# Kernel optimization log

Hardware: AMD Instinct MI355X
Metric: run time of the kernel (lower is better)

Reference implementation:

```python
import jax, jax.numpy as jnp
import numpy as np

B, S, D, H, E, N = 4, 1024, 1024, 4096, 1024, 8


def setup_inputs() -> dict:
    key = jax.random.key(0)
    ks = jax.random.split(key, 5)
    x = jax.random.normal(ks[0], (B, S, D), jnp.float32)
    # Learned parameters (Linear weights stored as [in, out] for x @ W)
    Wg = jax.random.normal(ks[1], (D, N), jnp.float32) * 0.02
    bg = jnp.zeros((N,), jnp.float32)
    W1 = jax.random.normal(ks[2], (N, D, H), jnp.float32) * 0.02
    b1 = jnp.zeros((N, H), jnp.float32)
    W2 = jax.random.normal(ks[3], (N, H, E), jnp.float32) * 0.02
    b2 = jnp.zeros((N, E), jnp.float32)
    return {"x": x, "Wg": Wg, "bg": bg, "W1": W1, "b1": b1,
            "W2": W2, "b2": b2, "num_experts_per_tok": 2}


def reference(x, Wg, bg, W1, b1, W2, b2, num_experts_per_tok):
    # Gating: softmax over experts
    gate_probs = jax.nn.softmax(x @ Wg + bg, axis=-1)            # [B,S,N]
    n_exp = gate_probs.shape[-1]
    # Top-k routing mask (indices are distinct, so summed one-hots == scatter of 1.0)
    _, topk_idx = jax.lax.top_k(gate_probs, num_experts_per_tok)  # [B,S,k]
    mask = jax.nn.one_hot(topk_idx, n_exp, dtype=gate_probs.dtype).sum(axis=-2)  # [B,S,N]
    gated = gate_probs * mask
    # F.normalize(p=1): divide by max(L1-norm, eps)
    gated = gated / jnp.maximum(jnp.sum(jnp.abs(gated), axis=-1, keepdims=True), 1e-12)
    # Dense all-expert FFN (matches torch.stack over ModuleList)
    h = jax.nn.relu(jnp.einsum('bsd,ndh->bsnh', x, W1) + b1)      # [B,S,N,H]
    expert_out = jnp.einsum('bsnh,nhe->bsne', h, W2) + b2          # [B,S,N,E]
    out = jnp.einsum('bsn,bsne->bse', gated, expert_out)           # [B,S,E]
    # Auxiliary load-balancing stats
    tokens = float(x.shape[0] * x.shape[1])
    importance = gate_probs.sum(axis=(0, 1)) / tokens              # [N]
    load = mask.sum(axis=(0, 1)) / tokens                          # [N]
    lb_loss = (n_exp * (importance * load).sum()).astype(out.dtype)
    return out, lb_loss, importance, load
```

## Files before the change

kernel.cpp:

```cpp
#include <hip/hip_runtime.h>

#define TOKENS 4096
#define DDIM 1024
#define HDIM 4096
#define EDIM 1024
#define NEXP 8
#define SLOTS (TOKENS * 2)
#define OUT_MAIN ((size_t)TOKENS * EDIM)
#define NKC2 2
#define KCHUNK2 (HDIM / NKC2)

typedef __bf16 bf16_t;
typedef bf16_t bf16x8 __attribute__((ext_vector_type(8)));
typedef float f32x4 __attribute__((ext_vector_type(4)));

__device__ __forceinline__ unsigned short f32_to_bf16(float f) {
  union { float f; unsigned u; } v; v.f = f;
  unsigned r = v.u + 0x7FFFu + ((v.u >> 16) & 1u);
  return (unsigned short)(r >> 16);
}

__device__ __forceinline__ void gload_lds16(const void* g, void* l) {
  __builtin_amdgcn_global_load_lds(
      (__attribute__((address_space(1))) void*)(g),
      (__attribute__((address_space(3))) void*)(l), 16, 0, 0);
}

__global__ __launch_bounds__(256) void gate_kernel(
    const float* __restrict__ x, const float* __restrict__ Wg,
    const float* __restrict__ bg, unsigned short* __restrict__ xb,
    int2* __restrict__ tok_e, float2* __restrict__ tok_w,
    float* __restrict__ probs) {
  const int wave = threadIdx.x >> 6;
  const int lane = threadIdx.x & 63;
  const int t = blockIdx.x * 4 + wave;
  const float4* xr = reinterpret_cast<const float4*>(x + (size_t)t * DDIM);
  ushort4* xbr = reinterpret_cast<ushort4*>(xb + (size_t)t * DDIM);

  float acc[NEXP];
#pragma unroll
  for (int n = 0; n < NEXP; n++) acc[n] = 0.f;

#pragma unroll
  for (int i = 0; i < 4; i++) {
    int d4 = lane + 64 * i;
    float4 xv = xr[d4];
    ushort4 o;
    o.x = f32_to_bf16(xv.x); o.y = f32_to_bf16(xv.y);
    o.z = f32_to_bf16(xv.z); o.w = f32_to_bf16(xv.w);
    xbr[d4] = o;
    const float* wrow = Wg + (size_t)d4 * 4 * NEXP;
#pragma unroll
    for (int n = 0; n < NEXP; n++)
      acc[n] += xv.x * wrow[n] + xv.y * wrow[NEXP + n] +
                xv.z * wrow[2 * NEXP + n] + xv.w * wrow[3 * NEXP + n];
  }
#pragma unroll
  for (int n = 0; n < NEXP; n++)
#pragma unroll
    for (int m = 32; m > 0; m >>= 1) acc[n] += __shfl_xor(acc[n], m, 64);

  if (lane == 0) {
    float p[NEXP];
    float mx = -1e30f;
#pragma unroll
    for (int n = 0; n < NEXP; n++) { p[n] = acc[n] + bg[n]; mx = fmaxf(mx, p[n]); }
    float s = 0.f;
#pragma unroll
    for (int n = 0; n < NEXP; n++) { p[n] = expf(p[n] - mx); s += p[n]; }
    float inv = 1.f / s;
#pragma unroll
    for (int n = 0; n < NEXP; n++) { p[n] *= inv; probs[(size_t)t * NEXP + n] = p[n]; }
    int e1 = 0; float p1 = p[0];
#pragma unroll
    for (int n = 1; n < NEXP; n++) if (p[n] > p1) { p1 = p[n]; e1 = n; }
    int e2 = (e1 == 0) ? 1 : 0; float p2 = p[e2];
#pragma unroll
    for (int n = 0; n < NEXP; n++) if (n != e1 && p[n] > p2) { p2 = p[n]; e2 = n; }
    float denom = p1 + p2;
    tok_e[t] = make_int2(e1, e2);
    tok_w[t] = make_float2(p1 / denom, p2 / denom);
  }
}

__global__ __launch_bounds__(1024) void route_kernel(
    const int2* __restrict__ tok_e, const float2* __restrict__ tok_w,
    int* __restrict__ offs_g, int* __restrict__ counts_g,
    int* __restrict__ token_ids, float* __restrict__ slot_w) {
  __shared__ int cnt[NEXP];
  __shared__ int offs[NEXP + 1];
  __shared__ int cur[NEXP];
  const int tid = threadIdx.x;
  if (tid < NEXP) cnt[tid] = 0;
  __syncthreads();
  int2 e[4]; float2 w[4];
#pragma unroll
  for (int i = 0; i < 4; i++) {
    int t = tid + 1024 * i;
    e[i] = tok_e[t]; w[i] = tok_w[t];
    atomicAdd(&cnt[e[i].x], 1);
    atomicAdd(&cnt[e[i].y], 1);
  }
  __syncthreads();
  if (tid == 0) {
    int s = 0;
#pragma unroll
    for (int n = 0; n < NEXP; n++) { offs[n] = s; cur[n] = s; s += cnt[n]; }
    offs[NEXP] = s;
  }
  __syncthreads();
  if (tid < NEXP) { offs_g[tid] = offs[tid]; counts_g[tid] = cnt[tid]; }
  if (tid == 0) offs_g[NEXP] = offs[NEXP];
#pragma unroll
  for (int i = 0; i < 4; i++) {
    int t = tid + 1024 * i;
    int s0 = atomicAdd(&cur[e[i].x], 1);
    token_ids[s0] = t; slot_w[s0] = w[i].x;
    int s1 = atomicAdd(&cur[e[i].y], 1);
    token_ids[s1] = t; slot_w[s1] = w[i].y;
  }
}

__global__ __launch_bounds__(256) void transpose_convert_kernel(
    const float* __restrict__ src, unsigned short* __restrict__ dst, int R, int C) {
  __shared__ float tile[64][65];
  const size_t mat = (size_t)R * C;
  const float* s = src + (size_t)blockIdx.z * mat;
  unsigned short* d = dst + (size_t)blockIdx.z * mat;
  int c0 = blockIdx.x * 64, r0 = blockIdx.y * 64;
  int tx = threadIdx.x & 15, ty = threadIdx.x >> 4;
#pragma unroll
  for (int i = 0; i < 4; i++) {
    int row = ty + 16 * i;
    float4 v = *reinterpret_cast<const float4*>(&s[(size_t)(r0 + row) * C + c0 + tx * 4]);
    tile[row][tx * 4 + 0] = v.x;
    tile[row][tx * 4 + 1] = v.y;
    tile[row][tx * 4 + 2] = v.z;
    tile[row][tx * 4 + 3] = v.w;
  }
  __syncthreads();
#pragma unroll
  for (int i = 0; i < 4; i++) {
    int col = ty + 16 * i;
    ushort4 o;
    o.x = f32_to_bf16(tile[tx * 4 + 0][col]);
    o.y = f32_to_bf16(tile[tx * 4 + 1][col]);
    o.z = f32_to_bf16(tile[tx * 4 + 2][col]);
    o.w = f32_to_bf16(tile[tx * 4 + 3][col]);
    *reinterpret_cast<ushort4*>(&d[(size_t)(c0 + col) * R + r0 + tx * 4]) = o;
  }
}

__global__ __launch_bounds__(256) void gemm1_kernel(
    const unsigned short* __restrict__ xb, const unsigned short* __restrict__ w1t,
    const float* __restrict__ b1, const int* __restrict__ token_ids,
    const int* __restrict__ offs, unsigned short* __restrict__ h) {
  const int e = blockIdx.z;
  const int off0 = offs[e];
  const int ne = offs[e + 1] - off0;
  const int mt = blockIdx.y;
  if (mt * 128 >= ne) return;
  const int nt = blockIdx.x;

  __shared__ unsigned short As[128 * 64];
  __shared__ unsigned short Bs[128 * 64];

  const int tid = threadIdx.x;
  const int lane = tid & 63;
  const int wave = tid >> 6;
  const int wm = (wave >> 1) * 64;
  const int wn = (wave & 1) * 64;

  const int prow = tid >> 3;
  const int krow = (tid & 7) ^ (prow & 7);
  const unsigned short* gA[4];
  const unsigned short* gB[4];
  const unsigned short* wbase = w1t + (size_t)e * HDIM * DDIM;
#pragma unroll
  for (int j = 0; j < 4; j++) {
    int row = prow + j * 32;
    int slot = off0 + min(mt * 128 + row, ne - 1);
    gA[j] = xb + (size_t)token_ids[slot] * DDIM + krow * 8;
    gB[j] = wbase + (size_t)(nt * 128 + row) * DDIM + krow * 8;
  }

  f32x4 acc[4][4];
#pragma unroll
  for (int i = 0; i < 4; i++)
#pragma unroll
    for (int j = 0; j < 4; j++) acc[i][j] = (f32x4)(0.f);

  const int frow = lane & 15;
  const int q = lane >> 4;

  for (int k0 = 0; k0 < DDIM; k0 += 64) {
    __syncthreads();
#pragma unroll
    for (int j = 0; j < 4; j++) {
      gload_lds16(gA[j] + k0, As + j * 2048 + wave * 512);
      gload_lds16(gB[j] + k0, Bs + j * 2048 + wave * 512);
    }
    __syncthreads();
#pragma unroll
    for (int kk = 0; kk < 2; kk++) {
      bf16x8 af[4], bfv[4];
#pragma unroll
      for (int mi = 0; mi < 4; mi++) {
        int row = wm + mi * 16 + frow;
        int k16 = (kk * 4 + q) ^ (row & 7);
        af[mi] = *reinterpret_cast<const bf16x8*>(&As[row * 64 + k16 * 8]);
      }
#pragma unroll
      for (int ni = 0; ni < 4; ni++) {
        int row = wn + ni * 16 + frow;
        int k16 = (kk * 4 + q) ^ (row & 7);
        bfv[ni] = *reinterpret_cast<const bf16x8*>(&Bs[row * 64 + k16 * 8]);
      }
#pragma unroll
      for (int mi = 0; mi < 4; mi++)
#pragma unroll
        for (int ni = 0; ni < 4; ni++)
          acc[mi][ni] = __builtin_amdgcn_mfma_f32_16x16x32_bf16(af[mi], bfv[ni], acc[mi][ni], 0, 0, 0);
    }
  }

  const float* b1e = b1 + (size_t)e * HDIM + nt * 128;
  const int r4 = (lane >> 4) * 4;
  const int cb = lane & 15;
#pragma unroll
  for (int mi = 0; mi < 4; mi++) {
#pragma unroll
    for (int r = 0; r < 4; r++) {
      int grow = mt * 128 + wm + mi * 16 + r4 + r;
      if (grow < ne) {
        unsigned short* hr = h + (size_t)(off0 + grow) * HDIM + nt * 128;
#pragma unroll
        for (int ni = 0; ni < 4; ni++) {
          int col = wn + ni * 16 + cb;
          float v = acc[mi][ni][r] + b1e[col];
          hr[col] = f32_to_bf16(fmaxf(v, 0.f));
        }
      }
    }
  }
}

__global__ __launch_bounds__(256) void gemm2_kernel(
    const unsigned short* __restrict__ h, const unsigned short* __restrict__ w2t,
    const float* __restrict__ b2, const int* __restrict__ token_ids,
    const float* __restrict__ slot_w, const int* __restrict__ offs,
    float* __restrict__ out) {
  const int ez = blockIdx.z;
  const int e = ez >> 1;
  const int kc = ez & 1;
  const int off0 = offs[e];
  const int ne = offs[e + 1] - off0;
  const int mt = blockIdx.y;
  if (mt * 128 >= ne) return;
  const int nt = blockIdx.x;

  __shared__ unsigned short As[128 * 64];
  __shared__ unsigned short Bs[128 * 64];

  const int tid = threadIdx.x;
  const int lane = tid & 63;
  const int wave = tid >> 6;
  const int wm = (wave >> 1) * 64;
  const int wn = (wave & 1) * 64;

  const int prow = tid >> 3;
  const int krow = (tid & 7) ^ (prow & 7);
  const unsigned short* gA[4];
  const unsigned short* gB[4];
  const unsigned short* wbase = w2t + (size_t)e * EDIM * HDIM;
#pragma unroll
  for (int j = 0; j < 4; j++) {
    int row = prow + j * 32;
    int slot = off0 + min(mt * 128 + row, ne - 1);
    gA[j] = h + (size_t)slot * HDIM + krow * 8;
    gB[j] = wbase + (size_t)(nt * 128 + row) * HDIM + krow * 8;
  }

  f32x4 acc[4][4];
#pragma unroll
  for (int i = 0; i < 4; i++)
#pragma unroll
    for (int j = 0; j < 4; j++) acc[i][j] = (f32x4)(0.f);

  const int frow = lane & 15;
  const int q = lane >> 4;

  for (int k0 = kc * KCHUNK2; k0 < (kc + 1) * KCHUNK2; k0 += 64) {
    __syncthreads();
#pragma unroll
    for (int j = 0; j < 4; j++) {
      gload_lds16(gA[j] + k0, As + j * 2048 + wave * 512);
      gload_lds16(gB[j] + k0, Bs + j * 2048 + wave * 512);
    }
    __syncthreads();
#pragma unroll
    for (int kk = 0; kk < 2; kk++) {
      bf16x8 af[4], bfv[4];
#pragma unroll
      for (int mi = 0; mi < 4; mi++) {
        int row = wm + mi * 16 + frow;
        int k16 = (kk * 4 + q) ^ (row & 7);
        af[mi] = *reinterpret_cast<const bf16x8*>(&As[row * 64 + k16 * 8]);
      }
#pragma unroll
      for (int ni = 0; ni < 4; ni++) {
        int row = wn + ni * 16 + frow;
        int k16 = (kk * 4 + q) ^ (row & 7);
        bfv[ni] = *reinterpret_cast<const bf16x8*>(&Bs[row * 64 + k16 * 8]);
      }
#pragma unroll
      for (int mi = 0; mi < 4; mi++)
#pragma unroll
        for (int ni = 0; ni < 4; ni++)
          acc[mi][ni] = __builtin_amdgcn_mfma_f32_16x16x32_bf16(af[mi], bfv[ni], acc[mi][ni], 0, 0, 0);
    }
  }

  const float* b2e = b2 + (size_t)e * EDIM + nt * 128;
  const int r4 = (lane >> 4) * 4;
  const int cb = lane & 15;
#pragma unroll
  for (int mi = 0; mi < 4; mi++) {
#pragma unroll
    for (int r = 0; r < 4; r++) {
      int grow = mt * 128 + wm + mi * 16 + r4 + r;
      if (grow < ne) {
        int slot = off0 + grow;
        int tokid = token_ids[slot];
        float wgt = slot_w[slot];
        float* orow = out + (size_t)tokid * EDIM + nt * 128;
#pragma unroll
        for (int ni = 0; ni < 4; ni++) {
          int col = wn + ni * 16 + cb;
          float bias = (kc == 0) ? b2e[col] : 0.f;
          atomicAdd(&orow[col], (acc[mi][ni][r] + bias) * wgt);
        }
      }
    }
  }
}

__global__ __launch_bounds__(512) void stats_kernel(
    const float* __restrict__ probs, const int* __restrict__ counts,
    float* __restrict__ tail) {
  const int wave = threadIdx.x >> 6;
  const int lane = threadIdx.x & 63;
  float s = 0.f;
  for (int t = lane; t < TOKENS; t += 64) s += probs[(size_t)t * NEXP + wave];
#pragma unroll
  for (int m = 32; m > 0; m >>= 1) s += __shfl_xor(s, m, 64);
  __shared__ float imp_s[NEXP];
  if (lane == 0) imp_s[wave] = s / (float)TOKENS;
  __syncthreads();
  if (threadIdx.x == 0) {
    float lb = 0.f;
#pragma unroll
    for (int n = 0; n < NEXP; n++) {
      float imp = imp_s[n];
      float ld = (float)counts[n] / (float)TOKENS;
      tail[1 + n] = imp;
      tail[1 + NEXP + n] = ld;
      lb += imp * ld;
    }
    tail[0] = (float)NEXP * lb;
  }
}

extern "C" void kernel_launch(void* const* d_in, const int* in_sizes, int n_in,
                              void* d_out, int out_size, void* d_ws, size_t ws_size,
                              hipStream_t stream) {
  const float* x  = (const float*)d_in[0];
  const float* Wg = (const float*)d_in[1];
  const float* bg = (const float*)d_in[2];
  const float* W1 = (const float*)d_in[3];
  const float* b1 = (const float*)d_in[4];
  const float* W2 = (const float*)d_in[5];
  const float* b2 = (const float*)d_in[6];
  float* out = (float*)d_out;
  char* ws = (char*)d_ws;

  const size_t XB_OFF   = 0;
  const size_t W1T_OFF  = XB_OFF + (size_t)TOKENS * DDIM * 2;
  const size_t W2T_OFF  = W1T_OFF + (size_t)NEXP * DDIM * HDIM * 2;
  const size_t H_OFF    = W2T_OFF + (size_t)NEXP * HDIM * EDIM * 2;
  const size_t TOKE_OFF = H_OFF + (size_t)SLOTS * HDIM * 2;
  const size_t TOKW_OFF = TOKE_OFF + (size_t)TOKENS * sizeof(int2);
  const size_t TID_OFF  = TOKW_OFF + (size_t)TOKENS * sizeof(float2);
  const size_t SLW_OFF  = TID_OFF + (size_t)SLOTS * 4;
  const size_t PROB_OFF = SLW_OFF + (size_t)SLOTS * 4;
  const size_t META_OFF = PROB_OFF + (size_t)TOKENS * NEXP * 4;
  const size_t WS_NEED  = META_OFF + 64 * 4;
  if (ws_size < WS_NEED) return;

  unsigned short* xb   = (unsigned short*)(ws + XB_OFF);
  unsigned short* w1t  = (unsigned short*)(ws + W1T_OFF);
  unsigned short* w2t  = (unsigned short*)(ws + W2T_OFF);
  unsigned short* hbuf = (unsigned short*)(ws + H_OFF);
  int2*   tok_e = (int2*)(ws + TOKE_OFF);
  float2* tok_w = (float2*)(ws + TOKW_OFF);
  int*    tids  = (int*)(ws + TID_OFF);
  float*  slw   = (float*)(ws + SLW_OFF);
  float*  probs = (float*)(ws + PROB_OFF);
  int*    counts = (int*)(ws + META_OFF);
  int*    offs   = counts + 8;

  hipMemsetAsync(out, 0, (size_t)out_size * sizeof(float), stream);

  gate_kernel<<<TOKENS / 4, 256, 0, stream>>>(x, Wg, bg, xb, tok_e, tok_w, probs);
  route_kernel<<<1, 1024, 0, stream>>>(tok_e, tok_w, offs, counts, tids, slw);
  transpose_convert_kernel<<<dim3(HDIM / 64, DDIM / 64, NEXP), 256, 0, stream>>>(W1, w1t, DDIM, HDIM);
  transpose_convert_kernel<<<dim3(EDIM / 64, HDIM / 64, NEXP), 256, 0, stream>>>(W2, w2t, HDIM, EDIM);
  gemm1_kernel<<<dim3(HDIM / 128, SLOTS / 128, NEXP), 256, 0, stream>>>(xb, w1t, b1, tids, offs, hbuf);
  gemm2_kernel<<<dim3(EDIM / 128, SLOTS / 128, NEXP * NKC2), 256, 0, stream>>>(hbuf, w2t, b2, tids, slw, offs, out);
  stats_kernel<<<1, 512, 0, stream>>>(probs, counts, out + OUT_MAIN);
}
```

Baseline: 473.6 us.

## Double-buffer LDS tiles in both expert GEMM kernels to overlap loads with MFMA

Both grouped GEMM kernels now keep two shared-memory buffers for the A and B tiles. The next K-slice is issued with global_load_lds into the alternate buffer while MFMAs consume the current one, and there is one barrier per iteration instead of two. The aim is to hide global-load latency behind compute. LDS use per block doubles to 64KB, which may lower occupancy, and overlap relies on the async load completing before the barrier.

```diff
diff --git a/kernel.cpp b/kernel.cpp
--- a/kernel.cpp
+++ b/kernel.cpp
@@ -162,8 +162,8 @@
   if (mt * 128 >= ne) return;
   const int nt = blockIdx.x;
 
-  __shared__ unsigned short As[128 * 64];
-  __shared__ unsigned short Bs[128 * 64];
+  __shared__ unsigned short As[2][128 * 64];
+  __shared__ unsigned short Bs[2][128 * 64];
 
   const int tid = threadIdx.x;
   const int lane = tid & 63;
@@ -192,15 +192,25 @@
 
   const int frow = lane & 15;
   const int q = lane >> 4;
-
-  for (int k0 = 0; k0 < DDIM; k0 += 64) {
-    __syncthreads();
-#pragma unroll
-    for (int j = 0; j < 4; j++) {
-      gload_lds16(gA[j] + k0, As + j * 2048 + wave * 512);
-      gload_lds16(gB[j] + k0, Bs + j * 2048 + wave * 512);
-    }
-    __syncthreads();
+  const int NK = DDIM / 64;
+
+#pragma unroll
+  for (int j = 0; j < 4; j++) {
+    gload_lds16(gA[j], &As[0][j * 2048 + wave * 512]);
+    gload_lds16(gB[j], &Bs[0][j * 2048 + wave * 512]);
+  }
+  __syncthreads();
+
+  for (int t = 0; t < NK; t++) {
+    const int cur = t & 1;
+    if (t + 1 < NK) {
+      const int k1 = (t + 1) * 64;
+#pragma unroll
+      for (int j = 0; j < 4; j++) {
+        gload_lds16(gA[j] + k1, &As[cur ^ 1][j * 2048 + wave * 512]);
+        gload_lds16(gB[j] + k1, &Bs[cur ^ 1][j * 2048 + wave * 512]);
+      }
+    }
 #pragma unroll
     for (int kk = 0; kk < 2; kk++) {
       bf16x8 af[4], bfv[4];
@@ -208,13 +218,13 @@
       for (int mi = 0; mi < 4; mi++) {
         int row = wm + mi * 16 + frow;
         int k16 = (kk * 4 + q) ^ (row & 7);
-        af[mi] = *reinterpret_cast<const bf16x8*>(&As[row * 64 + k16 * 8]);
+        af[mi] = *reinterpret_cast<const bf16x8*>(&As[cur][row * 64 + k16 * 8]);
       }
 #pragma unroll
       for (int ni = 0; ni < 4; ni++) {
         int row = wn + ni * 16 + frow;
         int k16 = (kk * 4 + q) ^ (row & 7);
-        bfv[ni] = *reinterpret_cast<const bf16x8*>(&Bs[row * 64 + k16 * 8]);
+        bfv[ni] = *reinterpret_cast<const bf16x8*>(&Bs[cur][row * 64 + k16 * 8]);
       }
 #pragma unroll
       for (int mi = 0; mi < 4; mi++)
@@ -222,6 +232,7 @@
         for (int ni = 0; ni < 4; ni++)
           acc[mi][ni] = __builtin_amdgcn_mfma_f32_16x16x32_bf16(af[mi], bfv[ni], acc[mi][ni], 0, 0, 0);
     }
+    __syncthreads();
   }
 
   const float* b1e = b1 + (size_t)e * HDIM + nt * 128;
@@ -259,8 +270,8 @@
   if (mt * 128 >= ne) return;
   const int nt = blockIdx.x;
 
-  __shared__ unsigned short As[128 * 64];
-  __shared__ unsigned short Bs[128 * 64];
+  __shared__ unsigned short As[2][128 * 64];
+  __shared__ unsigned short Bs[2][128 * 64];
 
   const int tid = threadIdx.x;
   const int lane = tid & 63;
@@ -273,12 +284,13 @@
   const unsigned short* gA[4];
   const unsigned short* gB[4];
   const unsigned short* wbase = w2t + (size_t)e * EDIM * HDIM;
+  const int kbase = kc * KCHUNK2;
 #pragma unroll
   for (int j = 0; j < 4; j++) {
     int row = prow + j * 32;
     int slot = off0 + min(mt * 128 + row, ne - 1);
-    gA[j] = h + (size_t)slot * HDIM + krow * 8;
-    gB[j] = wbase + (size_t)(nt * 128 + row) * HDIM + krow * 8;
+    gA[j] = h + (size_t)slot * HDIM + kbase + krow * 8;
+    gB[j] = wbase + (size_t)(nt * 128 + row) * HDIM + kbase + krow * 8;
   }
 
   f32x4 acc[4][4];
@@ -289,15 +301,25 @@
 
   const int frow = lane & 15;
   const int q = lane >> 4;
-
-  for (int k0 = kc * KCHUNK2; k0 < (kc + 1) * KCHUNK2; k0 += 64) {
-    __syncthreads();
-#pragma unroll
-    for (int j = 0; j < 4; j++) {
-      gload_lds16(gA[j] + k0, As + j * 2048 + wave * 512);
-      gload_lds16(gB[j] + k0, Bs + j * 2048 + wave * 512);
-    }
-    __syncthreads();
+  const int NK = KCHUNK2 / 64;
+
+#pragma unroll
+  for (int j = 0; j < 4; j++) {
+    gload_lds16(gA[j], &As[0][j * 2048 + wave * 512]);
+    gload_lds16(gB[j], &Bs[0][j * 2048 + wave * 512]);
+  }
+  __syncthreads();
+
+  for (int t = 0; t < NK; t++) {
+    const int cur = t & 1;
+    if (t + 1 < NK) {
+      const int k1 = (t + 1) * 64;
+#pragma unroll
+      for (int j = 0; j < 4; j++) {
+        gload_lds16(gA[j] + k1, &As[cur ^ 1][j * 2048 + wave * 512]);
+        gload_lds16(gB[j] + k1, &Bs[cur ^ 1][j * 2048 + wave * 512]);
+      }
+    }
 #pragma unroll
     for (int kk = 0; kk < 2; kk++) {
       bf16x8 af[4], bfv[4];
@@ -305,13 +327,13 @@
       for (int mi = 0; mi < 4; mi++) {
         int row = wm + mi * 16 + frow;
         int k16 = (kk * 4 + q) ^ (row & 7);
-        af[mi] = *reinterpret_cast<const bf16x8*>(&As[row * 64 + k16 * 8]);
+        af[mi] = *reinterpret_cast<const bf16x8*>(&As[cur][row * 64 + k16 * 8]);
       }
 #pragma unroll
       for (int ni = 0; ni < 4; ni++) {
         int row = wn + ni * 16 + frow;
         int k16 = (kk * 4 + q) ^ (row & 7);
-        bfv[ni] = *reinterpret_cast<const bf16x8*>(&Bs[row * 64 + k16 * 8]);
+        bfv[ni] = *reinterpret_cast<const bf16x8*>(&Bs[cur][row * 64 + k16 * 8]);
       }
 #pragma unroll
       for (int mi = 0; mi < 4; mi++)
@@ -319,6 +341,7 @@
         for (int ni = 0; ni < 4; ni++)
           acc[mi][ni] = __builtin_amdgcn_mfma_f32_16x16x32_bf16(af[mi], bfv[ni], acc[mi][ni], 0, 0, 0);
     }
+    __syncthreads();
   }
 
   const float* b2e = b2 + (size_t)e * EDIM + nt * 128;
```

Measured after the change: 495.0 us. +4.5%, slower.

## Replace gemm2 atomic scatter with per-slot slabs and a combine kernel

Applied to the files above, without the earlier changes.

gemm2 now writes weighted per-slot partial results with plain stores into two split-K slabs, and a new combine kernel gathers each token's two slots and two K-chunks into the output. This removes the fp32 atomicAdd scatter and the output memset, and makes the result order-deterministic. It costs an extra ~64MB of slab writes and reads plus one more launch. Launch bounds with min 4 blocks per SM were also added to both GEMMs, which may restrict registers.

```diff
diff --git a/kernel.cpp b/kernel.cpp
--- a/kernel.cpp
+++ b/kernel.cpp
@@ -9,6 +9,7 @@
 #define OUT_MAIN ((size_t)TOKENS * EDIM)
 #define NKC2 2
 #define KCHUNK2 (HDIM / NKC2)
+#define SLAB ((size_t)SLOTS * EDIM)
 
 typedef __bf16 bf16_t;
 typedef bf16_t bf16x8 __attribute__((ext_vector_type(8)));
@@ -86,7 +87,8 @@
 __global__ __launch_bounds__(1024) void route_kernel(
     const int2* __restrict__ tok_e, const float2* __restrict__ tok_w,
     int* __restrict__ offs_g, int* __restrict__ counts_g,
-    int* __restrict__ token_ids, float* __restrict__ slot_w) {
+    int* __restrict__ token_ids, float* __restrict__ slot_w,
+    int2* __restrict__ tok_slot) {
   __shared__ int cnt[NEXP];
   __shared__ int offs[NEXP + 1];
   __shared__ int cur[NEXP];
@@ -118,6 +120,7 @@
     token_ids[s0] = t; slot_w[s0] = w[i].x;
     int s1 = atomicAdd(&cur[e[i].y], 1);
     token_ids[s1] = t; slot_w[s1] = w[i].y;
+    tok_slot[t] = make_int2(s0, s1);
   }
 }
 
@@ -151,7 +154,8 @@
   }
 }
 
-__global__ __launch_bounds__(256) void gemm1_kernel(
+
+__global__ __launch_bounds__(256, 4) void gemm1_kernel(
     const unsigned short* __restrict__ xb, const unsigned short* __restrict__ w1t,
     const float* __restrict__ b1, const int* __restrict__ token_ids,
     const int* __restrict__ offs, unsigned short* __restrict__ h) {
@@ -245,11 +249,11 @@
   }
 }
 
-__global__ __launch_bounds__(256) void gemm2_kernel(
+__global__ __launch_bounds__(256, 4) void gemm2_kernel(
     const unsigned short* __restrict__ h, const unsigned short* __restrict__ w2t,
     const float* __restrict__ b2, const int* __restrict__ token_ids,
     const float* __restrict__ slot_w, const int* __restrict__ offs,
-    float* __restrict__ out) {
+    float* __restrict__ slot_out) {
   const int ez = blockIdx.z;
   const int e = ez >> 1;
   const int kc = ez & 1;
@@ -273,12 +277,13 @@
   const unsigned short* gA[4];
   const unsigned short* gB[4];
   const unsigned short* wbase = w2t + (size_t)e * EDIM * HDIM;
+  const int kbase = kc * KCHUNK2;
 #pragma unroll
   for (int j = 0; j < 4; j++) {
     int row = prow + j * 32;
     int slot = off0 + min(mt * 128 + row, ne - 1);
-    gA[j] = h + (size_t)slot * HDIM + krow * 8;
-    gB[j] = wbase + (size_t)(nt * 128 + row) * HDIM + krow * 8;
+    gA[j] = h + (size_t)slot * HDIM + kbase + krow * 8;
+    gB[j] = wbase + (size_t)(nt * 128 + row) * HDIM + kbase + krow * 8;
   }
 
   f32x4 acc[4][4];
@@ -290,7 +295,7 @@
   const int frow = lane & 15;
   const int q = lane >> 4;
 
-  for (int k0 = kc * KCHUNK2; k0 < (kc + 1) * KCHUNK2; k0 += 64) {
+  for (int k0 = 0; k0 < KCHUNK2; k0 += 64) {
     __syncthreads();
 #pragma unroll
     for (int j = 0; j < 4; j++) {
@@ -322,6 +327,7 @@
   }
 
   const float* b2e = b2 + (size_t)e * EDIM + nt * 128;
+  float* slab = slot_out + (size_t)kc * SLAB;
   const int r4 = (lane >> 4) * 4;
   const int cb = lane & 15;
 #pragma unroll
@@ -331,18 +337,31 @@
       int grow = mt * 128 + wm + mi * 16 + r4 + r;
       if (grow < ne) {
         int slot = off0 + grow;
-        int tokid = token_ids[slot];
         float wgt = slot_w[slot];
-        float* orow = out + (size_t)tokid * EDIM + nt * 128;
+        float* orow = slab + (size_t)slot * EDIM + nt * 128;
 #pragma unroll
         for (int ni = 0; ni < 4; ni++) {
           int col = wn + ni * 16 + cb;
           float bias = (kc == 0) ? b2e[col] : 0.f;
-          atomicAdd(&orow[col], (acc[mi][ni][r] + bias) * wgt);
+          orow[col] = (acc[mi][ni][r] + bias) * wgt;
         }
       }
     }
   }
+}
+
+__global__ __launch_bounds__(256) void combine_kernel(
+    const float* __restrict__ slot_out, const int2* __restrict__ tok_slot,
+    float* __restrict__ out) {
+  const int t = blockIdx.x;
+  const int c4 = threadIdx.x;
+  int2 s = tok_slot[t];
+  const f32x4* a0 = reinterpret_cast<const f32x4*>(slot_out + (size_t)s.x * EDIM);
+  const f32x4* a1 = reinterpret_cast<const f32x4*>(slot_out + (size_t)s.y * EDIM);
+  const f32x4* b0 = reinterpret_cast<const f32x4*>(slot_out + SLAB + (size_t)s.x * EDIM);
+  const f32x4* b1 = reinterpret_cast<const f32x4*>(slot_out + SLAB + (size_t)s.y * EDIM);
+  f32x4 v = a0[c4] + a1[c4] + b0[c4] + b1[c4];
+  reinterpret_cast<f32x4*>(out + (size_t)t * EDIM)[c4] = v;
 }
 
 __global__ __launch_bounds__(512) void stats_kernel(
@@ -388,9 +407,11 @@
   const size_t W1T_OFF  = XB_OFF + (size_t)TOKENS * DDIM * 2;
   const size_t W2T_OFF  = W1T_OFF + (size_t)NEXP * DDIM * HDIM * 2;
   const size_t H_OFF    = W2T_OFF + (size_t)NEXP * HDIM * EDIM * 2;
-  const size_t TOKE_OFF = H_OFF + (size_t)SLOTS * HDIM * 2;
+  const size_t SO_OFF   = H_OFF + (size_t)SLOTS * HDIM * 2;
+  const size_t TOKE_OFF = SO_OFF + (size_t)NKC2 * SLAB * 4;
   const size_t TOKW_OFF = TOKE_OFF + (size_t)TOKENS * sizeof(int2);
-  const size_t TID_OFF  = TOKW_OFF + (size_t)TOKENS * sizeof(float2);
+  const size_t TSLOT_OFF= TOKW_OFF + (size_t)TOKENS * sizeof(float2);
+  const size_t TID_OFF  = TSLOT_OFF + (size_t)TOKENS * sizeof(int2);
   const size_t SLW_OFF  = TID_OFF + (size_t)SLOTS * 4;
   const size_t PROB_OFF = SLW_OFF + (size_t)SLOTS * 4;
   const size_t META_OFF = PROB_OFF + (size_t)TOKENS * NEXP * 4;
@@ -401,21 +422,22 @@
   unsigned short* w1t  = (unsigned short*)(ws + W1T_OFF);
   unsigned short* w2t  = (unsigned short*)(ws + W2T_OFF);
   unsigned short* hbuf = (unsigned short*)(ws + H_OFF);
+  float*  slot_out = (float*)(ws + SO_OFF);
   int2*   tok_e = (int2*)(ws + TOKE_OFF);
   float2* tok_w = (float2*)(ws + TOKW_OFF);
+  int2*   tok_slot = (int2*)(ws + TSLOT_OFF);
   int*    tids  = (int*)(ws + TID_OFF);
   float*  slw   = (float*)(ws + SLW_OFF);
   float*  probs = (float*)(ws + PROB_OFF);
   int*    counts = (int*)(ws + META_OFF);
   int*    offs   = counts + 8;
 
-  hipMemsetAsync(out, 0, (size_t)out_size * sizeof(float), stream);
-
   gate_kernel<<<TOKENS / 4, 256, 0, stream>>>(x, Wg, bg, xb, tok_e, tok_w, probs);
-  route_kernel<<<1, 1024, 0, stream>>>(tok_e, tok_w, offs, counts, tids, slw);
+  route_kernel<<<1, 1024, 0, stream>>>(tok_e, tok_w, offs, counts, tids, slw, tok_slot);
   transpose_convert_kernel<<<dim3(HDIM / 64, DDIM / 64, NEXP), 256, 0, stream>>>(W1, w1t, DDIM, HDIM);
   transpose_convert_kernel<<<dim3(EDIM / 64, HDIM / 64, NEXP), 256, 0, stream>>>(W2, w2t, HDIM, EDIM);
   gemm1_kernel<<<dim3(HDIM / 128, SLOTS / 128, NEXP), 256, 0, stream>>>(xb, w1t, b1, tids, offs, hbuf);
-  gemm2_kernel<<<dim3(EDIM / 128, SLOTS / 128, NEXP * NKC2), 256, 0, stream>>>(hbuf, w2t, b2, tids, slw, offs, out);
+  gemm2_kernel<<<dim3(EDIM / 128, SLOTS / 128, NEXP * NKC2), 256, 0, stream>>>(hbuf, w2t, b2, tids, slw, offs, slot_out);
+  combine_kernel<<<TOKENS, 256, 0, stream>>>(slot_out, tok_slot, out);
   stats_kernel<<<1, 512, 0, stream>>>(probs, counts, out + OUT_MAIN);
 }
```

After: 588.3 us. +24.2%, slower.
